# Kernel optimization log

Measured on AMD Instinct MI355X. Metric: run time of the kernel, lower is better.

## Reference

```python
import jax, jax.numpy as jnp
import numpy as np

B, S, D, E, K = 2, 2048, 1024, 8, 2
DFF = 4 * D


def setup_inputs() -> dict:
    key = jax.random.key(0)
    ks = jax.random.split(key, 7)
    scale = 0.02
    return {
        "x": jax.random.normal(ks[0], (B, S, D), dtype=jnp.float32),
        "W1": jax.random.normal(ks[1], (E, D, DFF), dtype=jnp.float32) * scale,
        "b1": jnp.zeros((E, DFF), dtype=jnp.float32),
        "W2": jax.random.normal(ks[2], (E, DFF, D), dtype=jnp.float32) * scale,
        "b2": jnp.zeros((E, D), dtype=jnp.float32),
        "Wg": jax.random.normal(ks[3], (D, E), dtype=jnp.float32) * scale,
        "bg": jnp.zeros((E,), dtype=jnp.float32),
    }


def reference(x, W1, b1, W2, b2, Wg, bg):
    num_experts = W1.shape[0]
    # Gating: top-k logits -> softmax over the k selected experts
    gate_logits = jnp.einsum("bsd,de->bse", x, Wg) + bg          # [B,S,E]
    topk_w, topk_i = jax.lax.top_k(gate_logits, K)               # [B,S,K]
    topk_w = jax.nn.softmax(topk_w, axis=-1)
    # Per-expert combine weight (sum of routed weights, 0 if not routed)
    w = jnp.sum(
        jax.nn.one_hot(topk_i, num_experts, dtype=x.dtype) * topk_w[..., None],
        axis=-2,
    )                                                            # [B,S,E]
    # Faithful to original: every expert runs its full FFN over all tokens,
    # then outputs are masked by routing weights and summed.
    h = jax.nn.gelu(jnp.einsum("bsd,edf->bsef", x, W1) + b1, approximate=False)
    out = jnp.einsum("bsef,efd,bse->bsd", h, W2, w)
    out = out + jnp.einsum("bse,ed->bsd", w, b2)
    return out
```

## Files before the change

kernel.cpp:

```cpp
#include <hip/hip_runtime.h>
#include <math.h>

#define TOK 4096
#define D 1024
#define DFF 4096
#define NE 8
#define CAP 4096
#define YSLOTS 9216
#define GTOK 16

typedef _Float16 half4v __attribute__((ext_vector_type(4)));
typedef _Float16 half8v __attribute__((ext_vector_type(8)));
typedef float f32x4 __attribute__((ext_vector_type(4)));

#define GLOAD16(gp, lp) __builtin_amdgcn_global_load_lds( \
    (const __attribute__((address_space(1))) void*)(gp),  \
    (__attribute__((address_space(3))) void*)(lp), 16, 0, 0)

__device__ __forceinline__ float fast_gelu(float v) {
    float u = 0.7978845608f * (v + 0.044715f * v * v * v);
    float au = fabsf(u);
    float t = __expf(-2.f * au);
    float th = (1.f - t) / (1.f + t);
    th = u < 0.f ? -th : th;
    return 0.5f * v * (1.f + th);
}

__device__ __forceinline__ void mk_offs(const int* __restrict__ counts, int* offE) {
    offE[0] = 0;
#pragma unroll
    for (int k = 0; k < NE; ++k) offE[k + 1] = offE[k] + ((counts[k] + 127) & ~127);
}

__device__ __forceinline__ void tr_tile(const float* __restrict__ S,
                                        _Float16* __restrict__ T,
                                        int R, int C, int r0, int c0,
                                        char* smem, int tid) {
    float (*tile_t)[129] = (float(*)[129])smem;
    int cl = tid & 63;
    int rl = (tid >> 6) * 32;
#pragma unroll
    for (int k = 0; k < 32; ++k) {
        int r = rl + k;
        tile_t[cl][r] = S[(size_t)(r0 + r) * C + c0 + cl];
    }
    __syncthreads();
    int j = tid & 7;
#pragma unroll
    for (int p = 0; p < 2; ++p) {
        int c = p * 32 + (tid >> 3);
#pragma unroll
        for (int i = 0; i < 2; ++i) {
            int rb = i * 64 + j * 8;
            half8v h;
#pragma unroll
            for (int jj = 0; jj < 8; ++jj) h[jj] = (_Float16)tile_t[c][rb + jj];
            *(half8v*)(T + (size_t)(c0 + c) * R + r0 + rb) = h;
        }
    }
}


__global__ void k_gate_trw1(const float* __restrict__ x, const float* __restrict__ Wg,
                            const float* __restrict__ bg, int* __restrict__ counts,
                            int* __restrict__ tk_e, float* __restrict__ tk_w,
                            int* __restrict__ tk_pos, int* __restrict__ tok_list,
                            _Float16* __restrict__ xh,
                            const float* __restrict__ W1, _Float16* __restrict__ W1t) {
    __shared__ __align__(16) char smem[33024];
    int bid = blockIdx.x;
    int tid = threadIdx.x;
    if (bid >= 256) {
        int t = bid - 256;
        int e = t >> 9, xx = t & 511;
        tr_tile(W1 + (size_t)e * D * DFF, W1t + (size_t)e * DFF * D,
                D, DFF, (xx >> 6) * 128, (xx & 63) * 64, smem, tid);
        return;
    }
    int* s_e = (int*)smem;
    int* s_rank = (int*)(smem + 128);
    int* s_base = (int*)(smem + 256);
    int wid = tid >> 6, lane = tid & 63;
    int tbase = bid * GTOK;

    for (int i = 0; i < 4; ++i) {
        int tl = wid * 4 + i;
        int t = tbase + tl;
        const float* xr = x + (size_t)t * D;
        float a[NE];
#pragma unroll
        for (int e = 0; e < NE; ++e) a[e] = 0.f;
        for (int d = lane; d < D; d += 64) {
            float xv = xr[d];
            const float4 w0 = *(const float4*)(Wg + d * NE);
            const float4 w1 = *(const float4*)(Wg + d * NE + 4);
            a[0] += xv * w0.x; a[1] += xv * w0.y; a[2] += xv * w0.z; a[3] += xv * w0.w;
            a[4] += xv * w1.x; a[5] += xv * w1.y; a[6] += xv * w1.z; a[7] += xv * w1.w;
        }
#pragma unroll
        for (int j = 0; j < 2; ++j) {
            int ch = j * 64 + lane;
            float4 va = *(const float4*)(xr + ch * 8);
            float4 vb = *(const float4*)(xr + ch * 8 + 4);
            half8v h;
            h[0] = (_Float16)va.x; h[1] = (_Float16)va.y; h[2] = (_Float16)va.z; h[3] = (_Float16)va.w;
            h[4] = (_Float16)vb.x; h[5] = (_Float16)vb.y; h[6] = (_Float16)vb.z; h[7] = (_Float16)vb.w;
            *(half8v*)(xh + (size_t)t * D + ch * 8) = h;
        }
#pragma unroll
        for (int m = 1; m < 64; m <<= 1) {
#pragma unroll
            for (int e = 0; e < NE; ++e) a[e] += __shfl_xor(a[e], m, 64);
        }
        if (lane == 0) {
#pragma unroll
            for (int e = 0; e < NE; ++e) a[e] += bg[e];
            int i0 = 0;
#pragma unroll
            for (int e = 1; e < NE; ++e) if (a[e] > a[i0]) i0 = e;
            int i1 = (i0 == 0) ? 1 : 0;
#pragma unroll
            for (int e = 0; e < NE; ++e) if (e != i0 && a[e] > a[i1]) i1 = e;
            float ee = expf(a[i1] - a[i0]);
            float w0 = 1.f / (1.f + ee);
            float w1 = ee / (1.f + ee);
            tk_e[t * 2] = i0; tk_e[t * 2 + 1] = i1;
            tk_w[t * 2] = w0; tk_w[t * 2 + 1] = w1;
            s_e[tl * 2] = i0; s_e[tl * 2 + 1] = i1;
        }
    }
    __syncthreads();
    if (tid < 2 * GTOK) {
        int ei = s_e[tid];
        int r = 0;
#pragma unroll
        for (int j = 0; j < 2 * GTOK; ++j) r += (j < tid && s_e[j] == ei) ? 1 : 0;
        s_rank[tid] = r;
    } else if (tid >= 64 && tid < 64 + NE) {
        int e = tid - 64;
        int cnt = 0;
#pragma unroll
        for (int j = 0; j < 2 * GTOK; ++j) cnt += (s_e[j] == e) ? 1 : 0;
        s_base[e] = cnt ? atomicAdd(&counts[e], cnt) : 0;
    }
    __syncthreads();
    if (tid < 2 * GTOK) {
        int ei = s_e[tid];
        int t = tbase + (tid >> 1);
        int pos = s_base[ei] + s_rank[tid];
        tok_list[ei * CAP + pos] = t;
        tk_pos[t * 2 + (tid & 1)] = pos;
    }
}

__global__ __launch_bounds__(256, 4)
void k_ffn1_trw2(const _Float16* __restrict__ xh, const _Float16* __restrict__ W1t,
                 const float* __restrict__ b1, const int* __restrict__ counts,
                 const int* __restrict__ tok_list, _Float16* __restrict__ H,
                 const float* __restrict__ W2, _Float16* __restrict__ W2t) {
    __shared__ __align__(16) char smem[34816];
    int bid = blockIdx.x;
    int tid = threadIdx.x;
    if (bid >= 2304) {
        int t = bid - 2304;
        int e = t >> 9, xx = t & 511;
        tr_tile(W2 + (size_t)e * DFF * D, W2t + (size_t)e * D * DFF,
                DFF, D, (xx >> 4) * 128, (xx & 15) * 64, smem, tid);
        return;
    }
    int offE[NE + 1];
    mk_offs(counts, offE);
    int T = bid >> 5;
    if (T * 128 >= offE[NE]) return;
    int e = 0;
#pragma unroll
    for (int k = 1; k < NE; ++k) if (offE[k] <= T * 128) e = k;
    int row0 = T * 128 - offE[e];
    int n_e = counts[e];
    int bx = bid & 31;

    _Float16* As = (_Float16*)smem;
    _Float16* Bs = (_Float16*)(smem + 16384);
    int* s_tok = (int*)(smem + 32768);

    int lane = tid & 63, wid = tid >> 6;
    if (tid < 128) {
        int m = row0 + tid;
        s_tok[tid] = tok_list[e * CAP + (m < n_e ? m : n_e - 1)];
    }
    __syncthreads();

    int srow = lane >> 3, u = lane & 7;
    int wm = (wid >> 1) * 64, wn = (wid & 1) * 64;
    int cl = lane & 15, g = lane >> 4;
    int v8 = u ^ srow;
    int rbase = wid * 32 + srow;

    const _Float16* Abase = W1t + (size_t)e * DFF * D + (size_t)(bx * 128) * D + v8 * 8;
    const _Float16* bsrc[4];
#pragma unroll
    for (int i = 0; i < 4; ++i)
        bsrc[i] = xh + (size_t)s_tok[rbase + i * 8] * D + v8 * 8;

    f32x4 acc[4][4];
#pragma unroll
    for (int i = 0; i < 4; ++i)
#pragma unroll
        for (int j = 0; j < 4; ++j) acc[i][j] = (f32x4)0.f;

    for (int kt = 0; kt < D; kt += 64) {
#pragma unroll
        for (int i = 0; i < 4; ++i)
            GLOAD16(Abase + (size_t)(rbase + i * 8) * D + kt, As + (wid * 4 + i) * 512);
#pragma unroll
        for (int i = 0; i < 4; ++i)
            GLOAD16(bsrc[i] + kt, Bs + (wid * 4 + i) * 512);
        __syncthreads();
#pragma unroll
        for (int ks = 0; ks < 2; ++ks) {
            half8v aF[4], bF[4];
            int vv = ((ks * 4 + g) ^ (cl & 7)) * 8;
#pragma unroll
            for (int fm = 0; fm < 4; ++fm)
                aF[fm] = *(const half8v*)(As + (wm + fm * 16 + cl) * 64 + vv);
#pragma unroll
            for (int fn = 0; fn < 4; ++fn)
                bF[fn] = *(const half8v*)(Bs + (wn + fn * 16 + cl) * 64 + vv);
#pragma unroll
            for (int fm = 0; fm < 4; ++fm)
#pragma unroll
                for (int fn = 0; fn < 4; ++fn)
                    acc[fm][fn] = __builtin_amdgcn_mfma_f32_16x16x32_f16(aF[fm], bF[fn], acc[fm][fn], 0, 0, 0);
        }
        __syncthreads();
    }

    _Float16* Tile = (_Float16*)smem;
#pragma unroll
    for (int fm = 0; fm < 4; ++fm) {
        int featl = wm + fm * 16 + g * 4;
        float4 bv = *(const float4*)(b1 + e * DFF + bx * 128 + featl);
        float bb[4] = {bv.x, bv.y, bv.z, bv.w};
#pragma unroll
        for (int fn = 0; fn < 4; ++fn) {
            int sl = wn + fn * 16 + cl;
            half4v hv;
#pragma unroll
            for (int j = 0; j < 4; ++j) {
                float vv2 = acc[fm][fn][j] + bb[j];
                hv[j] = (_Float16)fast_gelu(vv2);
            }
            *(half4v*)(&Tile[sl * 136 + featl]) = hv;
        }
    }
    __syncthreads();
#pragma unroll
    for (int p = 0; p < 8; ++p) {
        int r = p * 16 + (tid >> 4);
        int c8 = (tid & 15) * 8;
        if (row0 + r < n_e)
            *(half8v*)(H + (size_t)(T * 128 + r) * DFF + bx * 128 + c8) =
                *(const half8v*)(&Tile[r * 136 + c8]);
    }
}

__global__ __launch_bounds__(256, 4)
void k_ffn2(const _Float16* __restrict__ H, const _Float16* __restrict__ W2t,
            const int* __restrict__ counts, _Float16* __restrict__ Yh) {
    int wg = blockIdx.x;
    int xcd = wg & 7, j = wg >> 3;
    int bx = j & 7;
    int tl = (j >> 3) % 9;
    int kh = j / 72;
    int T = xcd * 9 + tl;
    int offE[NE + 1];
    mk_offs(counts, offE);
    if (T * 128 >= offE[NE]) return;
    int e = 0;
#pragma unroll
    for (int k = 1; k < NE; ++k) if (offE[k] <= T * 128) e = k;
    int row0 = T * 128 - offE[e];
    int n_e = counts[e];

    __shared__ __align__(16) char smem[34816];
    _Float16* As = (_Float16*)smem;
    _Float16* Bs = (_Float16*)(smem + 16384);

    int tid = threadIdx.x, lane = tid & 63, wid = tid >> 6;
    int srow = lane >> 3, u = lane & 7;
    int wm = (wid >> 1) * 64, wn = (wid & 1) * 64;
    int cl = lane & 15, g = lane >> 4;
    int v8 = u ^ srow;
    int rbase = wid * 32 + srow;

    const _Float16* Abase = W2t + (size_t)e * D * DFF + (size_t)(bx * 128) * DFF + v8 * 8;
    const _Float16* Bbase = H + (size_t)(T * 128) * DFF + v8 * 8;

    f32x4 acc[4][4];
#pragma unroll
    for (int i = 0; i < 4; ++i)
#pragma unroll
        for (int j2 = 0; j2 < 4; ++j2) acc[i][j2] = (f32x4)0.f;

    int kt0 = kh * 2048, kt1 = kt0 + 2048;
    for (int kt = kt0; kt < kt1; kt += 64) {
#pragma unroll
        for (int i = 0; i < 4; ++i)
            GLOAD16(Abase + (size_t)(rbase + i * 8) * DFF + kt, As + (wid * 4 + i) * 512);
#pragma unroll
        for (int i = 0; i < 4; ++i)
            GLOAD16(Bbase + (size_t)(rbase + i * 8) * DFF + kt, Bs + (wid * 4 + i) * 512);
        __syncthreads();
#pragma unroll
        for (int ks = 0; ks < 2; ++ks) {
            half8v aF[4], bF[4];
            int vv = ((ks * 4 + g) ^ (cl & 7)) * 8;
#pragma unroll
            for (int fm = 0; fm < 4; ++fm)
                aF[fm] = *(const half8v*)(As + (wm + fm * 16 + cl) * 64 + vv);
#pragma unroll
            for (int fn = 0; fn < 4; ++fn)
                bF[fn] = *(const half8v*)(Bs + (wn + fn * 16 + cl) * 64 + vv);
#pragma unroll
            for (int fm = 0; fm < 4; ++fm)
#pragma unroll
                for (int fn = 0; fn < 4; ++fn)
                    acc[fm][fn] = __builtin_amdgcn_mfma_f32_16x16x32_f16(aF[fm], bF[fn], acc[fm][fn], 0, 0, 0);
        }
        __syncthreads();
    }

    _Float16* Tile = (_Float16*)smem;
#pragma unroll
    for (int fm = 0; fm < 4; ++fm) {
        int dl = wm + fm * 16 + g * 4;
#pragma unroll
        for (int fn = 0; fn < 4; ++fn) {
            int sl = wn + fn * 16 + cl;
            half4v hv;
#pragma unroll
            for (int j2 = 0; j2 < 4; ++j2) hv[j2] = (_Float16)acc[fm][fn][j2];
            *(half4v*)(&Tile[sl * 136 + dl]) = hv;
        }
    }
    __syncthreads();
#pragma unroll
    for (int p = 0; p < 8; ++p) {
        int r = p * 16 + (tid >> 4);
        int c8 = (tid & 15) * 8;
        if (row0 + r < n_e)
            *(half8v*)(Yh + ((size_t)kh * YSLOTS + T * 128 + r) * D + bx * 128 + c8) =
                *(const half8v*)(&Tile[r * 136 + c8]);
    }
}

__global__ void k_comb(const int* __restrict__ tk_e, const float* __restrict__ tk_w,
                       const int* __restrict__ tk_pos, const int* __restrict__ counts,
                       const _Float16* __restrict__ Yh, const float* __restrict__ b2,
                       float* __restrict__ out) {
    int idx = blockIdx.x * 256 + threadIdx.x;
    int t = idx >> 8;
    int d = (idx & 255) * 4;
    int offE[NE + 1];
    mk_offs(counts, offE);
    int e0 = tk_e[2 * t], e1 = tk_e[2 * t + 1];
    float w0 = tk_w[2 * t], w1 = tk_w[2 * t + 1];
    size_t s0 = offE[e0] + tk_pos[2 * t];
    size_t s1 = offE[e1] + tk_pos[2 * t + 1];
    half4v y00 = *(const half4v*)(Yh + s0 * D + d);
    half4v y01 = *(const half4v*)(Yh + ((size_t)YSLOTS + s0) * D + d);
    half4v y10 = *(const half4v*)(Yh + s1 * D + d);
    half4v y11 = *(const half4v*)(Yh + ((size_t)YSLOTS + s1) * D + d);
    float4 b20 = *(const float4*)(b2 + e0 * D + d);
    float4 b21 = *(const float4*)(b2 + e1 * D + d);
    float4 r;
    r.x = w0 * ((float)y00[0] + (float)y01[0] + b20.x) + w1 * ((float)y10[0] + (float)y11[0] + b21.x);
    r.y = w0 * ((float)y00[1] + (float)y01[1] + b20.y) + w1 * ((float)y10[1] + (float)y11[1] + b21.y);
    r.z = w0 * ((float)y00[2] + (float)y01[2] + b20.z) + w1 * ((float)y10[2] + (float)y11[2] + b21.z);
    r.w = w0 * ((float)y00[3] + (float)y01[3] + b20.w) + w1 * ((float)y10[3] + (float)y11[3] + b21.w);
    *(float4*)(out + (size_t)t * D + d) = r;
}

extern "C" void kernel_launch(void* const* d_in, const int* in_sizes, int n_in,
                              void* d_out, int out_size, void* d_ws, size_t ws_size,
                              hipStream_t stream) {
    const float* x  = (const float*)d_in[0];
    const float* W1 = (const float*)d_in[1];
    const float* b1 = (const float*)d_in[2];
    const float* W2 = (const float*)d_in[3];
    const float* b2 = (const float*)d_in[4];
    const float* Wg = (const float*)d_in[5];
    const float* bg = (const float*)d_in[6];
    float* out = (float*)d_out;

    char* ws = (char*)d_ws;
    int*   counts   = (int*)(ws);
    int*   tk_e     = (int*)(ws + 256);
    float* tk_w     = (float*)(ws + 33024);
    int*   tk_pos   = (int*)(ws + 65792);
    int*   tok_list = (int*)(ws + 98560);
    _Float16* xh    = (_Float16*)(ws + (1ull << 20));
    _Float16* W1t   = (_Float16*)(ws + (10ull << 20));
    _Float16* Yh    = (_Float16*)(ws + (10ull << 20));
    _Float16* W2t   = (_Float16*)(ws + (74ull << 20));
    _Float16* H     = (_Float16*)(ws + (138ull << 20));

    hipMemsetAsync(counts, 0, 64, stream);
    k_gate_trw1<<<256 + 4096, 256, 0, stream>>>(x, Wg, bg, counts, tk_e, tk_w, tk_pos,
                                                tok_list, xh, W1, W1t);
    k_ffn1_trw2<<<2304 + 4096, 256, 0, stream>>>(xh, W1t, b1, counts, tok_list,
                                                 H, W2, W2t);
    k_ffn2<<<8 * 144, 256, 0, stream>>>(H, W2t, counts, Yh);
    k_comb<<<(TOK * D / 4) / 256, 256, 0, stream>>>(tk_e, tk_w, tk_pos, counts, Yh, b2, out);
}
```

Before: 294.7 us.

## Shrink shared memory to 32KB via XOR swizzles and raise occupancy to 5 blocks

```diff
diff --git a/kernel.cpp b/kernel.cpp
--- a/kernel.cpp
+++ b/kernel.cpp
@@ -36,13 +36,13 @@
                                         _Float16* __restrict__ T,
                                         int R, int C, int r0, int c0,
                                         char* smem, int tid) {
-    float (*tile_t)[129] = (float(*)[129])smem;
+    float (*tile_t)[128] = (float(*)[128])smem;
     int cl = tid & 63;
     int rl = (tid >> 6) * 32;
 #pragma unroll
     for (int k = 0; k < 32; ++k) {
         int r = rl + k;
-        tile_t[cl][r] = S[(size_t)(r0 + r) * C + c0 + cl];
+        tile_t[cl][r ^ (cl & 31)] = S[(size_t)(r0 + r) * C + c0 + cl];
     }
     __syncthreads();
     int j = tid & 7;
@@ -54,20 +54,21 @@
             int rb = i * 64 + j * 8;
             half8v h;
 #pragma unroll
-            for (int jj = 0; jj < 8; ++jj) h[jj] = (_Float16)tile_t[c][rb + jj];
+            for (int jj = 0; jj < 8; ++jj) h[jj] = (_Float16)tile_t[c][(rb + jj) ^ (c & 31)];
             *(half8v*)(T + (size_t)(c0 + c) * R + r0 + rb) = h;
         }
     }
 }
 
 
-__global__ void k_gate_trw1(const float* __restrict__ x, const float* __restrict__ Wg,
-                            const float* __restrict__ bg, int* __restrict__ counts,
-                            int* __restrict__ tk_e, float* __restrict__ tk_w,
-                            int* __restrict__ tk_pos, int* __restrict__ tok_list,
-                            _Float16* __restrict__ xh,
-                            const float* __restrict__ W1, _Float16* __restrict__ W1t) {
-    __shared__ __align__(16) char smem[33024];
+__global__ __launch_bounds__(256, 5)
+void k_gate_trw1(const float* __restrict__ x, const float* __restrict__ Wg,
+                 const float* __restrict__ bg, int* __restrict__ counts,
+                 int* __restrict__ tk_e, float* __restrict__ tk_w,
+                 int* __restrict__ tk_pos, int* __restrict__ tok_list,
+                 _Float16* __restrict__ xh,
+                 const float* __restrict__ W1, _Float16* __restrict__ W1t) {
+    __shared__ __align__(16) char smem[32768];
     int bid = blockIdx.x;
     int tid = threadIdx.x;
     if (bid >= 256) {
@@ -153,12 +154,12 @@
     }
 }
 
-__global__ __launch_bounds__(256, 4)
+__global__ __launch_bounds__(256, 5)
 void k_ffn1_trw2(const _Float16* __restrict__ xh, const _Float16* __restrict__ W1t,
                  const float* __restrict__ b1, const int* __restrict__ counts,
                  const int* __restrict__ tok_list, _Float16* __restrict__ H,
                  const float* __restrict__ W2, _Float16* __restrict__ W2t) {
-    __shared__ __align__(16) char smem[34816];
+    __shared__ __align__(16) char smem[32768];
     int bid = blockIdx.x;
     int tid = threadIdx.x;
     if (bid >= 2304) {
@@ -181,15 +182,8 @@
 
     _Float16* As = (_Float16*)smem;
     _Float16* Bs = (_Float16*)(smem + 16384);
-    int* s_tok = (int*)(smem + 32768);
 
     int lane = tid & 63, wid = tid >> 6;
-    if (tid < 128) {
-        int m = row0 + tid;
-        s_tok[tid] = tok_list[e * CAP + (m < n_e ? m : n_e - 1)];
-    }
-    __syncthreads();
-
     int srow = lane >> 3, u = lane & 7;
     int wm = (wid >> 1) * 64, wn = (wid & 1) * 64;
     int cl = lane & 15, g = lane >> 4;
@@ -199,8 +193,11 @@
     const _Float16* Abase = W1t + (size_t)e * DFF * D + (size_t)(bx * 128) * D + v8 * 8;
     const _Float16* bsrc[4];
 #pragma unroll
-    for (int i = 0; i < 4; ++i)
-        bsrc[i] = xh + (size_t)s_tok[rbase + i * 8] * D + v8 * 8;
+    for (int i = 0; i < 4; ++i) {
+        int m = row0 + rbase + i * 8;
+        m = m < n_e ? m : n_e - 1;
+        bsrc[i] = xh + (size_t)tok_list[e * CAP + m] * D + v8 * 8;
+    }
 
     f32x4 acc[4][4];
 #pragma unroll
@@ -239,6 +236,7 @@
 #pragma unroll
     for (int fm = 0; fm < 4; ++fm) {
         int featl = wm + fm * 16 + g * 4;
+        int u16 = featl >> 3, off = featl & 7;
         float4 bv = *(const float4*)(b1 + e * DFF + bx * 128 + featl);
         float bb[4] = {bv.x, bv.y, bv.z, bv.w};
 #pragma unroll
@@ -250,21 +248,21 @@
                 float vv2 = acc[fm][fn][j] + bb[j];
                 hv[j] = (_Float16)fast_gelu(vv2);
             }
-            *(half4v*)(&Tile[sl * 136 + featl]) = hv;
+            *(half4v*)(&Tile[sl * 128 + ((u16 ^ (sl & 15)) << 3) + off]) = hv;
         }
     }
     __syncthreads();
 #pragma unroll
     for (int p = 0; p < 8; ++p) {
         int r = p * 16 + (tid >> 4);
-        int c8 = (tid & 15) * 8;
+        int uu = tid & 15;
         if (row0 + r < n_e)
-            *(half8v*)(H + (size_t)(T * 128 + r) * DFF + bx * 128 + c8) =
-                *(const half8v*)(&Tile[r * 136 + c8]);
-    }
-}
-
-__global__ __launch_bounds__(256, 4)
+            *(half8v*)(H + (size_t)(T * 128 + r) * DFF + bx * 128 + uu * 8) =
+                *(const half8v*)(&Tile[r * 128 + ((uu ^ (r & 15)) << 3)]);
+    }
+}
+
+__global__ __launch_bounds__(256, 5)
 void k_ffn2(const _Float16* __restrict__ H, const _Float16* __restrict__ W2t,
             const int* __restrict__ counts, _Float16* __restrict__ Yh) {
     int wg = blockIdx.x;
@@ -282,7 +280,7 @@
     int row0 = T * 128 - offE[e];
     int n_e = counts[e];
 
-    __shared__ __align__(16) char smem[34816];
+    __shared__ __align__(16) char smem[32768];
     _Float16* As = (_Float16*)smem;
     _Float16* Bs = (_Float16*)(smem + 16384);
 
@@ -334,23 +332,24 @@
 #pragma unroll
     for (int fm = 0; fm < 4; ++fm) {
         int dl = wm + fm * 16 + g * 4;
+        int u16 = dl >> 3, off = dl & 7;
 #pragma unroll
         for (int fn = 0; fn < 4; ++fn) {
             int sl = wn + fn * 16 + cl;
             half4v hv;
 #pragma unroll
             for (int j2 = 0; j2 < 4; ++j2) hv[j2] = (_Float16)acc[fm][fn][j2];
-            *(half4v*)(&Tile[sl * 136 + dl]) = hv;
+            *(half4v*)(&Tile[sl * 128 + ((u16 ^ (sl & 15)) << 3) + off]) = hv;
         }
     }
     __syncthreads();
 #pragma unroll
     for (int p = 0; p < 8; ++p) {
         int r = p * 16 + (tid >> 4);
-        int c8 = (tid & 15) * 8;
+        int uu = tid & 15;
         if (row0 + r < n_e)
-            *(half8v*)(Yh + ((size_t)kh * YSLOTS + T * 128 + r) * D + bx * 128 + c8) =
-                *(const half8v*)(&Tile[r * 136 + c8]);
+            *(half8v*)(Yh + ((size_t)kh * YSLOTS + T * 128 + r) * D + bx * 128 + uu * 8) =
+                *(const half8v*)(&Tile[r * 128 + ((uu ^ (r & 15)) << 3)]);
     }
 }
 
```

After: 589.5 us. 100% more time.
